# Performance work log

Measured on AMD Instinct MI355X. Metric: run time of the kernel, lower is better.

Reference implementation:

```python
import jax, jax.numpy as jnp
import numpy as np
import math

N_EMBD = 1024
N_HEAD = 16
HEAD_DIM = N_EMBD // N_HEAD
SEQ = 2048
BATCH = 2
EPS = 1e-5


def _gelu_tanh(x):
    c = math.sqrt(2.0 / math.pi)
    return 0.5 * x * (1.0 + jnp.tanh(c * (x + 0.044715 * x ** 3)))


def _layernorm(x, w, b):
    mean = jnp.mean(x, axis=-1, keepdims=True)
    var = jnp.mean(jnp.square(x - mean), axis=-1, keepdims=True)  # unbiased=False
    return (x - mean) / jnp.sqrt(var + EPS) * w + b


def setup_inputs() -> dict:
    key = jax.random.key(0)
    ks = jax.random.split(key, 8)
    D = N_EMBD
    s = 0.02
    return {
        "x": jax.random.normal(ks[0], (BATCH, SEQ, D), jnp.float32),
        "ln1_w": jnp.ones((D,), jnp.float32),
        "ln1_b": jnp.zeros((D,), jnp.float32),
        "w_qkv": jax.random.normal(ks[1], (D, 3 * D), jnp.float32) * s,
        "b_qkv": jnp.zeros((3 * D,), jnp.float32),
        "w_attn_proj": jax.random.normal(ks[2], (D, D), jnp.float32) * s,
        "b_attn_proj": jnp.zeros((D,), jnp.float32),
        "ln2_w": jnp.ones((D,), jnp.float32),
        "ln2_b": jnp.zeros((D,), jnp.float32),
        "w_fc": jax.random.normal(ks[3], (D, 4 * D), jnp.float32) * s,
        "b_fc": jnp.zeros((4 * D,), jnp.float32),
        "w_proj": jax.random.normal(ks[4], (4 * D, D), jnp.float32) * s,
        "b_proj": jnp.zeros((D,), jnp.float32),
    }


def reference(x, ln1_w, ln1_b, w_qkv, b_qkv, w_attn_proj, b_attn_proj,
              ln2_w, ln2_b, w_fc, b_fc, w_proj, b_proj):
    bs, T, D = x.shape
    # --- attention branch (pre-LN) ---
    h = _layernorm(x, ln1_w, ln1_b)
    qkv = h @ w_qkv + b_qkv                      # [B,T,3D]
    q, k, v = jnp.split(qkv, 3, axis=-1)
    q = q.reshape(bs, T, N_HEAD, HEAD_DIM).transpose(0, 2, 1, 3)  # [B,H,T,d]
    k = k.reshape(bs, T, N_HEAD, HEAD_DIM).transpose(0, 2, 1, 3)
    v = v.reshape(bs, T, N_HEAD, HEAD_DIM).transpose(0, 2, 1, 3)
    scores = jnp.einsum("bhqd,bhkd->bhqk", q, k) * (1.0 / math.sqrt(HEAD_DIM))
    causal = jnp.tril(jnp.ones((T, T), bool))
    scores = jnp.where(causal[None, None], scores, -jnp.inf)
    att = jax.nn.softmax(scores, axis=-1)
    ctx = jnp.einsum("bhqk,bhkd->bhqd", att, v)
    ctx = ctx.transpose(0, 2, 1, 3).reshape(bs, T, D)
    attn_out = ctx @ w_attn_proj + b_attn_proj
    x = x + attn_out
    # --- MLP branch (pre-LN) ---
    h = _layernorm(x, ln2_w, ln2_b)
    h = _gelu_tanh(h @ w_fc + b_fc)
    h = h @ w_proj + b_proj
    return x + h
```

## Files before the change

### kernel.cpp

```cpp
#include <hip/hip_runtime.h>

typedef unsigned short u16;
typedef __attribute__((ext_vector_type(8))) __bf16 bf16x8;
typedef __attribute__((ext_vector_type(8))) unsigned short ushort8;
typedef __attribute__((ext_vector_type(4))) float f32x4;

#define MFMA16(a, b, c) __builtin_amdgcn_mfma_f32_16x16x32_bf16((a), (b), (c), 0, 0, 0)

__device__ __forceinline__ u16 f2bf(float f) {
  union { __bf16 h; u16 u; } cv;
  cv.h = (__bf16)f;
  return cv.u;
}

__device__ __forceinline__ void async16(const u16* g, u16* l) {
  __builtin_amdgcn_global_load_lds(
      (const __attribute__((address_space(1))) void*)g,
      (__attribute__((address_space(3))) void*)l, 16, 0, 0);
}

__global__ __launch_bounds__(256)
void transpose_bf16(const float* __restrict__ W, u16* __restrict__ Wt, int K, int N) {
  __shared__ float t[32][33];
  const int n0 = blockIdx.x * 32, k0 = blockIdx.y * 32;
  const int tx = threadIdx.x, ty = threadIdx.y;
  #pragma unroll
  for (int i = 0; i < 32; i += 8)
    t[ty + i][tx] = W[(size_t)(k0 + ty + i) * N + n0 + tx];
  __syncthreads();
  #pragma unroll
  for (int i = 0; i < 32; i += 8)
    Wt[(size_t)(n0 + ty + i) * K + k0 + tx] = f2bf(t[tx][ty + i]);
}

__global__ __launch_bounds__(256)
void transpose_v(const u16* __restrict__ v, u16* __restrict__ vt) {
  __shared__ u16 t[64][72];
  const int bh = blockIdx.y, t0 = blockIdx.x * 64;
  const int tid = threadIdx.x;
  #pragma unroll
  for (int s = 0; s < 2; ++s) {
    const int idx = tid + s * 256;
    const int row = idx >> 3, ch = idx & 7;
    ushort8 d = *(const ushort8*)(v + ((size_t)bh * 2048 + t0 + row) * 64 + ch * 8);
    #pragma unroll
    for (int e = 0; e < 8; ++e) t[ch * 8 + e][row] = d[e];
  }
  __syncthreads();
  #pragma unroll
  for (int s = 0; s < 2; ++s) {
    const int idx = tid + s * 256;
    const int drow = idx >> 3, ch = idx & 7;
    ushort8 o = *(const ushort8*)(&t[drow][ch * 8]);
    *(ushort8*)(vt + ((size_t)bh * 64 + drow) * 2048 + t0 + ch * 8) = o;
  }
}

__global__ __launch_bounds__(256)
void ln_bf16(const float* __restrict__ X, const float* __restrict__ w,
             const float* __restrict__ bia, u16* __restrict__ out) {
  const int row = blockIdx.x, tid = threadIdx.x;
  const float4 v = ((const float4*)(X + (size_t)row * 1024))[tid];
  float s = v.x + v.y + v.z + v.w;
  float s2 = v.x * v.x + v.y * v.y + v.z * v.z + v.w * v.w;
  #pragma unroll
  for (int o = 32; o > 0; o >>= 1) { s += __shfl_down(s, o); s2 += __shfl_down(s2, o); }
  __shared__ float red[8];
  const int wv = tid >> 6, lane = tid & 63;
  if (lane == 0) { red[wv] = s; red[4 + wv] = s2; }
  __syncthreads();
  s = red[0] + red[1] + red[2] + red[3];
  s2 = red[4] + red[5] + red[6] + red[7];
  const float mean = s * (1.f / 1024.f);
  const float var = s2 * (1.f / 1024.f) - mean * mean;
  const float rstd = rsqrtf(var + 1e-5f);
  const float4 wv4 = ((const float4*)w)[tid];
  const float4 bv4 = ((const float4*)bia)[tid];
  ushort4 o;
  o.x = f2bf((v.x - mean) * rstd * wv4.x + bv4.x);
  o.y = f2bf((v.y - mean) * rstd * wv4.y + bv4.y);
  o.z = f2bf((v.z - mean) * rstd * wv4.z + bv4.z);
  o.w = f2bf((v.w - mean) * rstd * wv4.w + bv4.w);
  ((ushort4*)(out + (size_t)row * 1024))[tid] = o;
}

template <int MODE>
__global__ __launch_bounds__(256)
void gemm_bt(const u16* __restrict__ A, const u16* __restrict__ Bt,
             const float* __restrict__ bias, const float* __restrict__ resid,
             float* __restrict__ outF, u16* __restrict__ outB,
             u16* __restrict__ qo, u16* __restrict__ ko, u16* __restrict__ vo,
             int M, int N, int K, int kSlice) {
  __shared__ u16 As[128 * 64];
  __shared__ u16 Bs[128 * 64];
  const int tid = threadIdx.x;
  const int lane = tid & 63, wv = tid >> 6;
  const int l16 = lane & 15, quad = lane >> 4;
  const int wr = wv >> 1, wc = wv & 1;
  const int m0 = blockIdx.y * 128, n0 = blockIdx.x * 128;
  const int kBegin = blockIdx.z * kSlice, kEnd = kBegin + kSlice;
  const int srow = lane >> 3;
  const int sch = (lane & 7) ^ srow;

  f32x4 acc[4][4];
  const f32x4 fz = {0.f, 0.f, 0.f, 0.f};
  #pragma unroll
  for (int i = 0; i < 4; ++i)
    #pragma unroll
    for (int j = 0; j < 4; ++j) acc[i][j] = fz;

  for (int k0 = kBegin; k0 < kEnd; k0 += 64) {
    __syncthreads();
    #pragma unroll
    for (int s = 0; s < 4; ++s) {
      const int R = wv * 32 + s * 8;
      async16(A + (size_t)(m0 + R + srow) * K + k0 + sch * 8, As + R * 64);
      async16(Bt + (size_t)(n0 + R + srow) * K + k0 + sch * 8, Bs + R * 64);
    }
    __builtin_amdgcn_s_waitcnt(0xF70);
    __syncthreads();
    #pragma unroll
    for (int h = 0; h < 2; ++h) {
      bf16x8 af[4], bfr[4];
      #pragma unroll
      for (int i = 0; i < 4; ++i) {
        const int row = wr * 64 + i * 16 + l16;
        af[i] = *(const bf16x8*)(As + row * 64 + (((h * 4 + quad) ^ (l16 & 7)) * 8));
      }
      #pragma unroll
      for (int j = 0; j < 4; ++j) {
        const int row = wc * 64 + j * 16 + l16;
        bfr[j] = *(const bf16x8*)(Bs + row * 64 + (((h * 4 + quad) ^ (l16 & 7)) * 8));
      }
      #pragma unroll
      for (int i = 0; i < 4; ++i)
        #pragma unroll
        for (int j = 0; j < 4; ++j)
          acc[i][j] = MFMA16(af[i], bfr[j], acc[i][j]);
    }
  }

  #pragma unroll
  for (int i = 0; i < 4; ++i) {
    #pragma unroll
    for (int j = 0; j < 4; ++j) {
      const int col = n0 + wc * 64 + j * 16 + l16;
      #pragma unroll
      for (int r = 0; r < 4; ++r) {
        const int row = m0 + wr * 64 + i * 16 + quad * 4 + r;
        outF[(size_t)blockIdx.z * M * N + (size_t)row * N + col] = acc[i][j][r];
      }
    }
  }
}

template <int MODE>
__global__ __launch_bounds__(512)
void gemm256(const u16* __restrict__ A, const u16* __restrict__ Bt,
             const float* __restrict__ bias, u16* __restrict__ outB,
             u16* __restrict__ qo, u16* __restrict__ ko, u16* __restrict__ vo,
             int M, int N, int K) {
  __shared__ u16 As[4][256 * 32];
  __shared__ u16 Bs[4][256 * 32];
  const int tid = threadIdx.x;
  const int lane = tid & 63, wv = tid >> 6;
  const int l16 = lane & 15, quad = lane >> 4;
  const int wr = wv >> 2, wc = wv & 3;
  const int nwg = gridDim.x, cpx = nwg >> 3;
  const int bid = (int)blockIdx.x;
  const int swz = (bid & 7) * cpx + (bid >> 3);
  const int nbx = N >> 8;
  const int m0 = (swz / nbx) * 256, n0 = (swz % nbx) * 256;
  const int sR = lane >> 2;
  const int sc = lane & 3;

  f32x4 acc[8][4];
  const f32x4 fz = {0.f, 0.f, 0.f, 0.f};
  #pragma unroll
  for (int i = 0; i < 8; ++i)
    #pragma unroll
    for (int j = 0; j < 4; ++j) acc[i][j] = fz;

  auto stage = [&](int kt) {
    const int p = kt & 3;
    #pragma unroll
    for (int i = 0; i < 2; ++i) {
      const int r = i * 128 + wv * 16 + sR;
      const int ch = sc ^ ((r >> 1) & 3);
      async16(A + (size_t)(m0 + r) * K + kt * 32 + ch * 8,
              &As[p][(i * 128 + wv * 16) * 32]);
      async16(Bt + (size_t)(n0 + r) * K + kt * 32 + ch * 8,
              &Bs[p][(i * 128 + wv * 16) * 32]);
    }
  };
  auto ldf = [&](const u16* base, int r) {
    return *(const bf16x8*)(base + r * 32 + ((quad ^ ((r >> 1) & 3)) * 8));
  };

  const int nt = K >> 5;
  stage(0);
  stage(1);
  stage(2);
  __builtin_amdgcn_s_waitcnt(0xF78);
  __builtin_amdgcn_s_barrier();
  __builtin_amdgcn_sched_barrier(0);

  for (int kt = 0; kt < nt; ++kt) {
    if (kt + 3 < nt) stage(kt + 3);
    const u16* Ap = As[kt & 3];
    const u16* Bp = Bs[kt & 3];
    bf16x8 b[4];
    #pragma unroll
    for (int j = 0; j < 4; ++j) b[j] = ldf(Bp, wc * 64 + j * 16 + l16);
    __builtin_amdgcn_s_setprio(1);
    #pragma unroll
    for (int i = 0; i < 8; ++i) {
      bf16x8 a = ldf(Ap, wr * 128 + i * 16 + l16);
      #pragma unroll
      for (int j = 0; j < 4; ++j) acc[i][j] = MFMA16(a, b[j], acc[i][j]);
    }
    __builtin_amdgcn_s_setprio(0);
    if (kt + 3 < nt)
      __builtin_amdgcn_s_waitcnt(0xF78);
    else if (kt + 2 < nt)
      __builtin_amdgcn_s_waitcnt(0xF74);
    else if (kt + 1 < nt)
      __builtin_amdgcn_s_waitcnt(0xF70);
    if (kt + 1 < nt) {
      __builtin_amdgcn_s_barrier();
      __builtin_amdgcn_sched_barrier(0);
    }
  }

  #pragma unroll
  for (int i = 0; i < 8; ++i) {
    #pragma unroll
    for (int j = 0; j < 4; ++j) {
      const int col = n0 + wc * 64 + j * 16 + l16;
      const float bc = bias[col];
      #pragma unroll
      for (int r = 0; r < 4; ++r) {
        const int row = m0 + wr * 128 + i * 16 + quad * 4 + r;
        float v = acc[i][j][r] + bc;
        if (MODE == 0) {
          const int which = col >> 10, cc = col & 1023, hh = cc >> 6, dd = cc & 63;
          const int bb = row >> 11, t = row & 2047;
          const u16 bv = f2bf(v);
          const size_t o = ((size_t)(bb * 16 + hh) * 2048 + t) * 64 + dd;
          if (which == 0)
            qo[o] = bv;
          else if (which == 1)
            ko[o] = bv;
          else
            vo[o] = bv;
        } else {
          const float x3 = v * v * v;
          const float u = 0.7978845608028654f * (v + 0.044715f * x3);
          const float e = __expf(2.f * u);
          const float th = 1.f - 2.f / (e + 1.f);
          outB[(size_t)row * N + col] = f2bf(0.5f * v * (1.f + th));
        }
      }
    }
  }
}

__global__ __launch_bounds__(256)
void reduce2(const float* __restrict__ P, const float* __restrict__ resid,
             const float* __restrict__ bias, float* __restrict__ out, int MN, int N) {
  const int idx4 = blockIdx.x * 256 + threadIdx.x;
  const size_t s = (size_t)MN >> 2;
  const float4 a = ((const float4*)P)[idx4];
  const float4 b = ((const float4*)P)[idx4 + s];
  const float4 r = ((const float4*)resid)[idx4];
  const float4 bb = ((const float4*)bias)[idx4 & (N / 4 - 1)];
  float4 o;
  o.x = r.x + a.x + b.x + bb.x;
  o.y = r.y + a.y + b.y + bb.y;
  o.z = r.z + a.z + b.z + bb.z;
  o.w = r.w + a.w + b.w + bb.w;
  ((float4*)out)[idx4] = o;
}

__global__ __launch_bounds__(256)
void reduce2_ln(const float* __restrict__ P, const float* __restrict__ resid,
                const float* __restrict__ bias, const float* __restrict__ lw,
                const float* __restrict__ lb, float* __restrict__ out,
                u16* __restrict__ h2, int MN) {
  const int row = blockIdx.x, tid = threadIdx.x;
  const int idx4 = row * 256 + tid;
  const size_t s4 = (size_t)MN >> 2;
  const float4 a = ((const float4*)P)[idx4];
  const float4 b = ((const float4*)P)[idx4 + s4];
  const float4 r = ((const float4*)resid)[idx4];
  const float4 bb = ((const float4*)bias)[tid];
  float4 o;
  o.x = r.x + a.x + b.x + bb.x;
  o.y = r.y + a.y + b.y + bb.y;
  o.z = r.z + a.z + b.z + bb.z;
  o.w = r.w + a.w + b.w + bb.w;
  ((float4*)out)[idx4] = o;
  float s = o.x + o.y + o.z + o.w;
  float s2 = o.x * o.x + o.y * o.y + o.z * o.z + o.w * o.w;
  #pragma unroll
  for (int of = 32; of > 0; of >>= 1) { s += __shfl_down(s, of); s2 += __shfl_down(s2, of); }
  __shared__ float red[8];
  const int wv = tid >> 6, lane = tid & 63;
  if (lane == 0) { red[wv] = s; red[4 + wv] = s2; }
  __syncthreads();
  s = red[0] + red[1] + red[2] + red[3];
  s2 = red[4] + red[5] + red[6] + red[7];
  const float mean = s * (1.f / 1024.f);
  const float var = s2 * (1.f / 1024.f) - mean * mean;
  const float rstd = rsqrtf(var + 1e-5f);
  const float4 wv4 = ((const float4*)lw)[tid];
  const float4 bv4 = ((const float4*)lb)[tid];
  ushort4 ob;
  ob.x = f2bf((o.x - mean) * rstd * wv4.x + bv4.x);
  ob.y = f2bf((o.y - mean) * rstd * wv4.y + bv4.y);
  ob.z = f2bf((o.z - mean) * rstd * wv4.z + bv4.z);
  ob.w = f2bf((o.w - mean) * rstd * wv4.w + bv4.w);
  ((ushort4*)(h2 + (size_t)row * 1024))[tid] = ob;
}

typedef union { bf16x8 v; unsigned d[4]; } PFU;

__global__ __launch_bounds__(512)
void attn(const u16* __restrict__ Q, const u16* __restrict__ Kg,
          const u16* __restrict__ Vt, u16* __restrict__ ctx) {
  __shared__ u16 Ks[2][128 * 64];
  __shared__ u16 Vs[64 * 128];
  const int pair = blockIdx.x;
  const int qt0 = pair, qt1 = 15 - pair;
  const int bh = blockIdx.y;
  const int b = bh >> 4, h = bh & 15;
  const int tid = threadIdx.x;
  const int lane = tid & 63, wv = tid >> 6;
  const int l16 = lane & 15, quad = lane >> 4;
  const int rb = wv * 16;
  const float S2 = 0.18033688011112042f;
  const u16* Qb = Q + (size_t)bh * 2048 * 64;
  const u16* Kb = Kg + (size_t)bh * 2048 * 64;
  const u16* Vb = Vt + (size_t)bh * 64 * 2048;

  bf16x8 qf[2][2];
  #pragma unroll
  for (int t = 0; t < 2; ++t)
    #pragma unroll
    for (int c = 0; c < 2; ++c)
      qf[t][c] = *(const bf16x8*)(Qb + (size_t)((t ? qt1 : qt0) * 128 + rb + l16) * 64 +
                                  c * 32 + quad * 8);

  f32x4 octx[2][4];
  const f32x4 fz = {0.f, 0.f, 0.f, 0.f};
  #pragma unroll
  for (int t = 0; t < 2; ++t)
    #pragma unroll
    for (int jd = 0; jd < 4; ++jd) octx[t][jd] = fz;
  float mi[2] = {-1e30f, -1e30f};
  float li[2] = {0.f, 0.f};

  const int kRow = lane >> 3, kCh = (lane & 7) ^ ((lane >> 3) & 7);
  const int vRow = lane >> 4;
  auto stageK = [&](int kt, int buf) {
    #pragma unroll
    for (int s = 0; s < 2; ++s) {
      const int R = wv * 16 + s * 8;
      async16(Kb + (size_t)(kt * 128 + R + kRow) * 64 + kCh * 8, &Ks[buf][R * 64]);
    }
  };
  auto stageV = [&](int kt) {
    #pragma unroll
    for (int s = 0; s < 2; ++s) {
      const int D = wv * 8 + s * 4;
      const int dd = D + vRow;
      const int sch = (lane & 15) ^ (dd & 15);
      async16(Vb + (size_t)dd * 2048 + kt * 128 + sch * 8, &Vs[D * 128]);
    }
  };

  const int ps0 = l16 + 16 * (2 * (quad & 1) + (quad >> 1));
  const int ps1 = ps0 ^ 16;
  const bool qlo = (quad & 1) == 0;
  const bool qh2 = (quad >> 1) == 0;

  auto qkt = [&](const u16* KsC, bf16x8* qv, f32x4* sa) {
    __builtin_amdgcn_s_setprio(1);
    #pragma unroll
    for (int j = 0; j < 8; ++j) {
      const int key7 = l16 & 7;
      bf16x8 kf0 = *(const bf16x8*)(KsC + (16 * j + l16) * 64 + ((quad ^ key7) * 8));
      bf16x8 kf1 = *(const bf16x8*)(KsC + (16 * j + l16) * 64 + (((4 + quad) ^ key7) * 8));
      sa[j] = MFMA16(kf1, qv[1], MFMA16(kf0, qv[0], fz));
    }
    __builtin_amdgcn_s_setprio(0);
  };

  auto smx = [&](f32x4* sa, int t, int kt, int qt, PFU* pf) {
    if (kt == qt) {
      const int rg = rb + l16;
      #pragma unroll
      for (int j = 0; j < 8; ++j)
        #pragma unroll
        for (int r = 0; r < 4; ++r)
          if (j * 16 + quad * 4 + r > rg) sa[j][r] = -1e30f;
    }
    float mj[8];
    #pragma unroll
    for (int j = 0; j < 8; ++j)
      mj[j] = fmaxf(fmaxf(sa[j][0], sa[j][1]), fmaxf(sa[j][2], sa[j][3]));
    float mx = fmaxf(fmaxf(fmaxf(mj[0], mj[1]), fmaxf(mj[2], mj[3])),
                     fmaxf(fmaxf(mj[4], mj[5]), fmaxf(mj[6], mj[7])));
    mx = fmaxf(mx, __shfl_xor(mx, 16));
    mx = fmaxf(mx, __shfl_xor(mx, 32));
    mx *= S2;
    const bool skip = (__all(mx - mi[t] <= 8.f) != 0);
    float mn = mi[t];
    float al = 1.f;
    if (!skip) {
      mn = fmaxf(mi[t], mx);
      al = __builtin_amdgcn_exp2f(mi[t] - mn);
      mi[t] = mn;
    }
    float r0 = 0.f, r1 = 0.f, r2 = 0.f, r3 = 0.f;
    unsigned w01[8], w23[8];
    #pragma unroll
    for (int j = 0; j < 8; ++j) {
      const float p0 = __builtin_amdgcn_exp2f(sa[j][0] * S2 - mn);
      const float p1 = __builtin_amdgcn_exp2f(sa[j][1] * S2 - mn);
      const float p2 = __builtin_amdgcn_exp2f(sa[j][2] * S2 - mn);
      const float p3 = __builtin_amdgcn_exp2f(sa[j][3] * S2 - mn);
      r0 += p0; r1 += p1; r2 += p2; r3 += p3;
      w01[j] = (unsigned)f2bf(p0) | ((unsigned)f2bf(p1) << 16);
      w23[j] = (unsigned)f2bf(p2) | ((unsigned)f2bf(p3) << 16);
    }
    float rs = (r0 + r1) + (r2 + r3);
    rs += __shfl_xor(rs, 16);
    rs += __shfl_xor(rs, 32);
    if (skip) {
      li[t] += rs;
    } else {
      li[t] = li[t] * al + rs;
      #pragma unroll
      for (int r = 0; r < 4; ++r) {
        const float alr = __shfl(al, quad * 4 + r);
        #pragma unroll
        for (int jd = 0; jd < 4; ++jd) octx[t][jd][r] *= alr;
      }
    }
    #pragma unroll
    for (int c = 0; c < 4; ++c) {
      const unsigned a0 = qlo ? w01[2 * c] : w01[2 * c + 1];
      const unsigned a1 = qlo ? w01[2 * c + 1] : w01[2 * c];
      const unsigned b0 = qlo ? w23[2 * c] : w23[2 * c + 1];
      const unsigned b1 = qlo ? w23[2 * c + 1] : w23[2 * c];
      const unsigned r00 = (unsigned)__shfl((int)a0, ps0);
      const unsigned r01 = (unsigned)__shfl((int)a1, ps1);
      const unsigned r10 = (unsigned)__shfl((int)b0, ps0);
      const unsigned r11 = (unsigned)__shfl((int)b1, ps1);
      pf[c].d[0] = qh2 ? r00 : r01;
      pf[c].d[2] = qh2 ? r01 : r00;
      pf[c].d[1] = qh2 ? r10 : r11;
      pf[c].d[3] = qh2 ? r11 : r10;
    }
  };

  auto pv = [&](PFU* pf, f32x4* oc) {
    __builtin_amdgcn_s_setprio(1);
    #pragma unroll
    for (int c = 0; c < 4; ++c) {
      #pragma unroll
      for (int jd = 0; jd < 4; ++jd) {
        const int dd = jd * 16 + l16;
        bf16x8 vf = *(const bf16x8*)(Vs + dd * 128 + (((c * 4 + quad) ^ (dd & 15)) * 8));
        oc[jd] = MFMA16(pf[c].v, vf, oc[jd]);
      }
    }
    __builtin_amdgcn_s_setprio(0);
  };

  stageK(0, 0);
  __builtin_amdgcn_s_waitcnt(0xF70);
  __syncthreads();

  for (int kt = 0; kt <= qt1; ++kt) {
    const int cur = kt & 1;
    stageV(kt);
    if (kt < qt1) stageK(kt + 1, cur ^ 1);
    const bool both = (kt <= qt0);
    const u16* KsC = Ks[cur];

    PFU pf0[4], pf1[4];
    {
      f32x4 sa[8];
      if (both) {
        qkt(KsC, qf[0], sa);
        smx(sa, 0, kt, qt0, pf0);
      }
      qkt(KsC, qf[1], sa);
      smx(sa, 1, kt, qt1, pf1);
    }

    __builtin_amdgcn_s_waitcnt(0xF70);
    __syncthreads();

    if (both) pv(pf0, octx[0]);
    pv(pf1, octx[1]);
    __syncthreads();
  }

  #pragma unroll
  for (int t = 0; t < 2; ++t) {
    const int qt = t ? qt1 : qt0;
    #pragma unroll
    for (int r = 0; r < 4; ++r) {
      const float lr = __builtin_amdgcn_rcpf(__shfl(li[t], quad * 4 + r));
      const int rowg = qt * 128 + rb + quad * 4 + r;
      #pragma unroll
      for (int jd = 0; jd < 4; ++jd) {
        const int col = h * 64 + jd * 16 + l16;
        ctx[((size_t)b * 2048 + rowg) * 1024 + col] = f2bf(octx[t][jd][r] * lr);
      }
    }
  }
}

extern "C" void kernel_launch(void* const* d_in, const int* in_sizes, int n_in,
                              void* d_out, int out_size, void* d_ws, size_t ws_size,
                              hipStream_t stream) {
  (void)in_sizes; (void)n_in; (void)out_size; (void)ws_size;
  const float* x      = (const float*)d_in[0];
  const float* ln1_w  = (const float*)d_in[1];
  const float* ln1_b  = (const float*)d_in[2];
  const float* w_qkv  = (const float*)d_in[3];
  const float* b_qkv  = (const float*)d_in[4];
  const float* w_attn = (const float*)d_in[5];
  const float* b_attn = (const float*)d_in[6];
  const float* ln2_w  = (const float*)d_in[7];
  const float* ln2_b  = (const float*)d_in[8];
  const float* w_fc   = (const float*)d_in[9];
  const float* b_fc   = (const float*)d_in[10];
  const float* w_proj = (const float*)d_in[11];
  const float* b_proj = (const float*)d_in[12];
  float* out = (float*)d_out;

  char* ws = (char*)d_ws;
  size_t off = 0;
  auto alloc = [&](size_t n) {
    char* p = ws + off;
    off += (n + 255) & ~(size_t)255;
    return p;
  };
  u16* h1     = (u16*)alloc(4096ull * 1024 * 2);
  u16* wqkvT  = (u16*)alloc(3072ull * 1024 * 2);
  u16* wattnT = (u16*)alloc(1024ull * 1024 * 2);
  u16* wfcT   = (u16*)alloc(4096ull * 1024 * 2);
  u16* wprojT = (u16*)alloc(1024ull * 4096 * 2);
  u16* q      = (u16*)alloc(4096ull * 1024 * 2);
  u16* k      = (u16*)alloc(4096ull * 1024 * 2);
  u16* vT     = (u16*)alloc(4096ull * 1024 * 2);
  u16* ctxb   = (u16*)alloc(4096ull * 1024 * 2);
  float* out1 = (float*)alloc(4096ull * 1024 * 4);
  u16* h2     = (u16*)alloc(4096ull * 1024 * 2);
  u16* fco    = (u16*)alloc(4096ull * 4096 * 2);

  u16* vtmp = ctxb;
  float* apP = (float*)fco;
  float* projP = (float*)q;

  const dim3 tb(32, 8);
  transpose_bf16<<<dim3(3072 / 32, 1024 / 32), tb, 0, stream>>>(w_qkv, wqkvT, 1024, 3072);
  transpose_bf16<<<dim3(1024 / 32, 1024 / 32), tb, 0, stream>>>(w_attn, wattnT, 1024, 1024);
  transpose_bf16<<<dim3(4096 / 32, 1024 / 32), tb, 0, stream>>>(w_fc, wfcT, 1024, 4096);
  transpose_bf16<<<dim3(1024 / 32, 4096 / 32), tb, 0, stream>>>(w_proj, wprojT, 4096, 1024);

  ln_bf16<<<4096, 256, 0, stream>>>(x, ln1_w, ln1_b, h1);

  gemm256<0><<<dim3(192), 512, 0, stream>>>(h1, wqkvT, b_qkv, nullptr, q, k, vtmp,
                                            4096, 3072, 1024);

  transpose_v<<<dim3(32, 32), 256, 0, stream>>>(vtmp, vT);

  attn<<<dim3(8, 32), 512, 0, stream>>>(q, k, vT, ctxb);

  gemm_bt<4><<<dim3(8, 32, 2), 256, 0, stream>>>(ctxb, wattnT, b_attn, nullptr, apP, nullptr,
                                                 nullptr, nullptr, nullptr, 4096, 1024, 1024, 512);
  reduce2_ln<<<4096, 256, 0, stream>>>(apP, x, b_attn, ln2_w, ln2_b, out1, h2, 4096 * 1024);

  gemm256<2><<<dim3(256), 512, 0, stream>>>(h2, wfcT, b_fc, fco, nullptr, nullptr, nullptr,
                                            4096, 4096, 1024);

  gemm_bt<4><<<dim3(8, 32, 2), 256, 0, stream>>>(fco, wprojT, b_proj, nullptr, projP, nullptr,
                                                 nullptr, nullptr, nullptr, 4096, 1024, 4096, 2048);

  reduce2<<<4096, 256, 0, stream>>>(projP, out1, b_proj, out, 4096 * 1024, 1024);
}
```

Measured before the change: 363.4 us.

## Restructure 256x256 GEMM into double-buffered K=64 tiles with phased staging

Rewrites the main loop of the large GEMM kernel so it moves from a 4-stage ring of K=32 tiles to two LDS buffers of K=64 tiles. Each tile is split into four compute phases of 32 rows, and half-tile async loads are interleaved between phases. The LDS XOR swizzle is widened to 8 chunks to match. The goal is to overlap global-to-LDS transfers with MFMA work at a finer grain and to cut loop and barrier overhead per K step. In exchange it adds more barriers per tile and uses hand-tuned waitcnt values that must line up exactly with the number of outstanding loads.

```diff
diff --git a/kernel.cpp b/kernel.cpp
--- a/kernel.cpp
+++ b/kernel.cpp
@@ -160,19 +160,19 @@
              const float* __restrict__ bias, u16* __restrict__ outB,
              u16* __restrict__ qo, u16* __restrict__ ko, u16* __restrict__ vo,
              int M, int N, int K) {
-  __shared__ u16 As[4][256 * 32];
-  __shared__ u16 Bs[4][256 * 32];
+  __shared__ u16 Al[2][256 * 64];
+  __shared__ u16 Bl[2][256 * 64];
   const int tid = threadIdx.x;
   const int lane = tid & 63, wv = tid >> 6;
   const int l16 = lane & 15, quad = lane >> 4;
-  const int wr = wv >> 2, wc = wv & 3;
+  const int wm = wv >> 2, wn = wv & 3;
   const int nwg = gridDim.x, cpx = nwg >> 3;
   const int bid = (int)blockIdx.x;
   const int swz = (bid & 7) * cpx + (bid >> 3);
   const int nbx = N >> 8;
   const int m0 = (swz / nbx) * 256, n0 = (swz % nbx) * 256;
-  const int sR = lane >> 2;
-  const int sc = lane & 3;
+  const int stR = lane >> 3, stC = lane & 7;
+  const int stSrc = stC ^ stR;
 
   f32x4 acc[8][4];
   const f32x4 fz = {0.f, 0.f, 0.f, 0.f};
@@ -181,66 +181,89 @@
     #pragma unroll
     for (int j = 0; j < 4; ++j) acc[i][j] = fz;
 
-  auto stage = [&](int kt) {
-    const int p = kt & 3;
-    #pragma unroll
-    for (int i = 0; i < 2; ++i) {
-      const int r = i * 128 + wv * 16 + sR;
-      const int ch = sc ^ ((r >> 1) & 3);
-      async16(A + (size_t)(m0 + r) * K + kt * 32 + ch * 8,
-              &As[p][(i * 128 + wv * 16) * 32]);
-      async16(Bt + (size_t)(n0 + r) * K + kt * 32 + ch * 8,
-              &Bs[p][(i * 128 + wv * 16) * 32]);
-    }
-  };
-  auto ldf = [&](const u16* base, int r) {
-    return *(const bf16x8*)(base + r * 32 + ((quad ^ ((r >> 1) & 3)) * 8));
-  };
-
-  const int nt = K >> 5;
-  stage(0);
-  stage(1);
-  stage(2);
-  __builtin_amdgcn_s_waitcnt(0xF78);
-  __builtin_amdgcn_s_barrier();
-  __builtin_amdgcn_sched_barrier(0);
-
-  for (int kt = 0; kt < nt; ++kt) {
-    if (kt + 3 < nt) stage(kt + 3);
-    const u16* Ap = As[kt & 3];
-    const u16* Bp = Bs[kt & 3];
-    bf16x8 b[4];
-    #pragma unroll
-    for (int j = 0; j < 4; ++j) b[j] = ldf(Bp, wc * 64 + j * 16 + l16);
+  auto stageH = [&](const u16* G, int rowBase, u16* L, int kt, int h) {
+    #pragma unroll
+    for (int s = 0; s < 2; ++s) {
+      const int r = wv * 8 + stR + s * 64;
+      async16(G + (size_t)(rowBase + h * 128 + r) * K + kt * 64 + stSrc * 8,
+              L + (h * 128 + r) * 64);
+    }
+  };
+  auto ldf = [&](const u16* base, int row, int sel) {
+    return *(const bf16x8*)(base + row * 64 + ((sel ^ (row & 7)) * 8));
+  };
+
+  bf16x8 bfr[4][2];
+  auto phase = [&](const u16* Ab, const u16* Bb, int q, bool loadB, bool vm4) {
+    if (loadB) {
+      #pragma unroll
+      for (int j4 = 0; j4 < 4; ++j4)
+        #pragma unroll
+        for (int h = 0; h < 2; ++h)
+          bfr[j4][h] = ldf(Bb, wn * 64 + j4 * 16 + l16, h * 4 + quad);
+    }
+    bf16x8 a[2][2];
+    #pragma unroll
+    for (int rt = 0; rt < 2; ++rt)
+      #pragma unroll
+      for (int h = 0; h < 2; ++h)
+        a[rt][h] = ldf(Ab, wm * 128 + q * 32 + rt * 16 + l16, h * 4 + quad);
+    __builtin_amdgcn_s_barrier();
+    __builtin_amdgcn_s_waitcnt(0xC07F);
+    __builtin_amdgcn_sched_barrier(0);
     __builtin_amdgcn_s_setprio(1);
     #pragma unroll
-    for (int i = 0; i < 8; ++i) {
-      bf16x8 a = ldf(Ap, wr * 128 + i * 16 + l16);
-      #pragma unroll
-      for (int j = 0; j < 4; ++j) acc[i][j] = MFMA16(a, b[j], acc[i][j]);
-    }
+    for (int rt = 0; rt < 2; ++rt)
+      #pragma unroll
+      for (int j4 = 0; j4 < 4; ++j4)
+        #pragma unroll
+        for (int h = 0; h < 2; ++h)
+          acc[2 * q + rt][j4] = MFMA16(a[rt][h], bfr[j4][h], acc[2 * q + rt][j4]);
     __builtin_amdgcn_s_setprio(0);
-    if (kt + 3 < nt)
-      __builtin_amdgcn_s_waitcnt(0xF78);
-    else if (kt + 2 < nt)
-      __builtin_amdgcn_s_waitcnt(0xF74);
-    else if (kt + 1 < nt)
-      __builtin_amdgcn_s_waitcnt(0xF70);
-    if (kt + 1 < nt) {
-      __builtin_amdgcn_s_barrier();
-      __builtin_amdgcn_sched_barrier(0);
-    }
+    if (vm4) __builtin_amdgcn_s_waitcnt(0xF74);
+    __builtin_amdgcn_s_barrier();
+    __builtin_amdgcn_sched_barrier(0);
+  };
+
+  const int nt = K >> 6;
+  stageH(A, m0, Al[0], 0, 0);
+  stageH(A, m0, Al[0], 0, 1);
+  stageH(Bt, n0, Bl[0], 0, 0);
+  stageH(Bt, n0, Bl[0], 0, 1);
+  stageH(Bt, n0, Bl[1], 1, 0);
+  stageH(Bt, n0, Bl[1], 1, 1);
+  __builtin_amdgcn_s_waitcnt(0xF70);
+  __syncthreads();
+
+  for (int j = 0; j < (nt >> 1); ++j) {
+    const int ta = 2 * j, tb = 2 * j + 1;
+    stageH(A, m0, Al[1], tb, 0);
+    phase(Al[0], Bl[0], 0, true, false);
+    stageH(A, m0, Al[1], tb, 1);
+    if (ta + 2 < nt) stageH(Bt, n0, Bl[0], ta + 2, 0);
+    phase(Al[0], Bl[0], 1, false, false);
+    if (ta + 2 < nt) stageH(Bt, n0, Bl[0], ta + 2, 1);
+    phase(Al[0], Bl[0], 2, false, false);
+    phase(Al[0], Bl[0], 3, false, true);
+    if (ta + 2 < nt) stageH(A, m0, Al[0], ta + 2, 0);
+    phase(Al[1], Bl[1], 0, true, false);
+    if (ta + 2 < nt) stageH(A, m0, Al[0], ta + 2, 1);
+    phase(Al[1], Bl[1], 1, false, false);
+    if (tb + 2 < nt) stageH(Bt, n0, Bl[1], tb + 2, 0);
+    phase(Al[1], Bl[1], 2, false, false);
+    if (tb + 2 < nt) stageH(Bt, n0, Bl[1], tb + 2, 1);
+    phase(Al[1], Bl[1], 3, false, true);
   }
 
   #pragma unroll
   for (int i = 0; i < 8; ++i) {
     #pragma unroll
     for (int j = 0; j < 4; ++j) {
-      const int col = n0 + wc * 64 + j * 16 + l16;
+      const int col = n0 + wn * 64 + j * 16 + l16;
       const float bc = bias[col];
       #pragma unroll
       for (int r = 0; r < 4; ++r) {
-        const int row = m0 + wr * 128 + i * 16 + quad * 4 + r;
+        const int row = m0 + wm * 128 + i * 16 + quad * 4 + r;
         float v = acc[i][j][r] + bc;
         if (MODE == 0) {
           const int which = col >> 10, cc = col & 1023, hh = cc >> 6, dd = cc & 63;
```

Result: faster. 354.2 us (-2.5%).
